# Performance work log

Hardware: AMD Instinct MI355X
Metric: run time of the kernel (lower is better)

## Reference

```python
import jax, jax.numpy as jnp
from jax import lax
import numpy as np

B, S, D_CTX = 32, 384, 300
H = 600            # hard-coded in the torch module (torch.zeros([1, 600]))
IN = D_CTX + 3     # context + 3-dim BIO tag embedding


def setup_inputs() -> dict:
    key = jax.random.key(0)
    ks = jax.random.split(key, 12)
    sc = lambda *sh: 1.0 / np.sqrt(sh[-1])
    return {
        "context": jax.random.normal(ks[0], (B, S, D_CTX), jnp.float32),
        "answer_tags": jax.random.randint(ks[1], (B, 1, S), 0, 3),
        "bio_emb": jax.random.normal(ks[2], (3, 3), jnp.float32),
        # GRUCell params (torch layout: W_ih [3H, IN], W_hh [3H, H])
        "W_ih": jax.random.normal(ks[3], (3 * H, IN), jnp.float32) * sc(3 * H, IN),
        "b_ih": jax.random.normal(ks[4], (3 * H,), jnp.float32) * 0.01,
        "W_hh": jax.random.normal(ks[5], (3 * H, H), jnp.float32) * sc(3 * H, H),
        "b_hh": jax.random.normal(ks[6], (3 * H,), jnp.float32) * 0.01,
        "W_lin": jax.random.normal(ks[7], (2 * H, 2 * H), jnp.float32) * sc(2 * H, 2 * H),
        "b_lin": jnp.zeros((2 * H,), jnp.float32),
        "W_g": jax.random.normal(ks[8], (2 * H, 4 * H), jnp.float32) * sc(2 * H, 4 * H),
        "b_g": jnp.zeros((2 * H,), jnp.float32),
        "W_f": jax.random.normal(ks[9], (2 * H, 4 * H), jnp.float32) * sc(2 * H, 4 * H),
        "b_f": jnp.zeros((2 * H,), jnp.float32),
    }


def _gru_scan(xs, W_ih, b_ih, W_hh, b_hh):
    # xs: [T, IN]; hidden carries across ALL steps (the torch code never resets
    # the hidden state between batch elements -- faithful quirk).
    gi_all = xs @ W_ih.T + b_ih            # [T, 3H] precomputed input projections

    def step(h, gi):
        gh = h @ W_hh.T + b_hh             # [3H]
        ir, iz, inn = jnp.split(gi, 3)
        hr, hz, hn = jnp.split(gh, 3)
        r = jax.nn.sigmoid(ir + hr)
        z = jax.nn.sigmoid(iz + hz)
        n = jnp.tanh(inn + r * hn)
        h_new = (1.0 - z) * n + z * h
        return h_new, h_new

    h0 = jnp.zeros((H,), xs.dtype)
    h_last, hs = lax.scan(step, h0, gi_all)
    return h_last, hs                      # [H], [T, H]


def reference(context, answer_tags, bio_emb, W_ih, b_ih, W_hh, b_hh,
              W_lin, b_lin, W_g, b_g, W_f, b_f):
    b, s, _ = context.shape
    tags = bio_emb[answer_tags[:, 0, :]]                    # [B, S, 3]
    emb = jnp.concatenate([tags, context], axis=-1)          # [B, S, IN]

    # Forward direction: one continuous scan over all B*S steps (hidden not reset).
    h_f, fwd = _gru_scan(emb.reshape(b * s, -1), W_ih, b_ih, W_hh, b_hh)
    forward_states = fwd.reshape(b, s, H)

    # Backward direction: words reversed within each batch element; the torch
    # code stores backward_states[b, w] = state after processing word S-1-w.
    h_b, bwd = _gru_scan(emb[:, ::-1, :].reshape(b * s, -1), W_ih, b_ih, W_hh, b_hh)
    backward_states = bwd.reshape(b, s, H)

    all_h = jnp.concatenate([forward_states, backward_states], axis=-1)  # [B,S,2H]

    # calc_attention: the inner state_idx loop OVERWRITES attn[b,:,:] each
    # iteration, so only the LAST state (index S-1) survives, broadcast over S.
    hs = all_h[:, -1, :]                                     # [B, 2H]
    q = hs @ W_lin.T + b_lin                                 # [B, 2H]
    scores = jax.nn.softmax(jnp.einsum('bd,bsd->bs', q, all_h), axis=-1)
    ctx = jnp.einsum('bs,bsd->bd', scores, all_h)            # [B, 2H]
    cat = jnp.concatenate([ctx, hs], axis=-1)                # [B, 4H]
    g = jax.nn.sigmoid(cat @ W_g.T + b_g)
    f = jnp.tanh(cat @ W_f.T + b_f)
    gated = g * f + (1.0 - g) * hs                           # [B, 2H]
    attn = jnp.broadcast_to(gated[:, None, :], (b, s, 2 * H))

    final = jnp.concatenate([h_f, h_b])[None, :]             # [1, 2H]
    return final, attn
```

## Files before the change

kernel.cpp:

```cpp
#include <hip/hip_runtime.h>
#include <math.h>

#define TT    12288
#define HH    600
#define GG    1800
#define INP   303
#define INP_P 304
#define BB    32
#define SS    384
#define D2    1200
#define D4    2400

#define NWG  75
#define JPW  8
#define ROWS 24

#define SENT 0xAAAAAAAAu

#define EMB_OFF    0ull
#define WP_OFF     3735552ull
#define GI_OFF     4282752ull
#define HS_OFF     26403808ull
#define Q_OFF      26442208ull
#define CTX_OFF    26480608ull
#define GATED_OFF  26519008ull
#define P_OFF      0ull

__global__ void build_emb(const float* __restrict__ ctx, const int* __restrict__ tags,
                          const float* __restrict__ bio, float* __restrict__ emb) {
    int idx = blockIdx.x * 256 + threadIdx.x;
    if (idx >= TT * INP_P) return;
    int row = idx / INP_P;
    int c = idx - row * INP_P;
    float v;
    if (c < 3)        v = bio[tags[row] * 3 + c];
    else if (c < INP) v = ctx[(size_t)row * 300 + (c - 3)];
    else              v = 0.f;
    emb[idx] = v;
}

__global__ void pad_wih(const float* __restrict__ W, float* __restrict__ Wp) {
    int idx = blockIdx.x * 256 + threadIdx.x;
    if (idx >= GG * INP_P) return;
    int r = idx / INP_P, c = idx - r * INP_P;
    Wp[idx] = (c < INP) ? W[(size_t)r * INP + c] : 0.f;
}

__global__ __launch_bounds__(256) void gemm_gi(const float* __restrict__ A,
                                               const float* __restrict__ Bw,
                                               const float* __restrict__ bias,
                                               float* __restrict__ C) {
    __shared__ float As[16][68];
    __shared__ float Bs[16][68];
    const int tid = threadIdx.x;
    const int bm = blockIdx.x, bn = blockIdx.y;
    const int tx = tid & 15, ty = tid >> 4;
    const int lm = tid >> 2;
    const int lk = (tid & 3) * 4;
    const int gbase = bn * 64;
    float acc[4][4] = {};
    for (int k0 = 0; k0 < INP_P; k0 += 16) {
        float4 av = *(const float4*)(A + (size_t)(bm * 64 + lm) * INP_P + k0 + lk);
        int grow = gbase + lm;
        float4 bv = make_float4(0.f, 0.f, 0.f, 0.f);
        if (grow < GG) bv = *(const float4*)(Bw + (size_t)grow * INP_P + k0 + lk);
        As[lk + 0][lm] = av.x; As[lk + 1][lm] = av.y; As[lk + 2][lm] = av.z; As[lk + 3][lm] = av.w;
        Bs[lk + 0][lm] = bv.x; Bs[lk + 1][lm] = bv.y; Bs[lk + 2][lm] = bv.z; Bs[lk + 3][lm] = bv.w;
        __syncthreads();
#pragma unroll
        for (int kk = 0; kk < 16; ++kk) {
            float4 a4 = *(const float4*)&As[kk][tx * 4];
            float4 b4 = *(const float4*)&Bs[kk][ty * 4];
            acc[0][0] += a4.x * b4.x; acc[0][1] += a4.x * b4.y; acc[0][2] += a4.x * b4.z; acc[0][3] += a4.x * b4.w;
            acc[1][0] += a4.y * b4.x; acc[1][1] += a4.y * b4.y; acc[1][2] += a4.y * b4.z; acc[1][3] += a4.y * b4.w;
            acc[2][0] += a4.z * b4.x; acc[2][1] += a4.z * b4.y; acc[2][2] += a4.z * b4.z; acc[2][3] += a4.z * b4.w;
            acc[3][0] += a4.w * b4.x; acc[3][1] += a4.w * b4.y; acc[3][2] += a4.w * b4.z; acc[3][3] += a4.w * b4.w;
        }
        __syncthreads();
    }
    int g0 = gbase + ty * 4;
    if (g0 < GG) {
        float4 bi4 = *(const float4*)(bias + g0);
#pragma unroll
        for (int i = 0; i < 4; ++i) {
            float4 v = make_float4(acc[i][0] + bi4.x, acc[i][1] + bi4.y,
                                   acc[i][2] + bi4.z, acc[i][3] + bi4.w);
            *(float4*)(C + (size_t)(bm * 64 + tx * 4 + i) * GG + g0) = v;
        }
    }
}

__global__ __launch_bounds__(256) void gru_scan(const float* __restrict__ gi,
                                                const float* __restrict__ Whh,
                                                const float* __restrict__ bhh,
                                                float* __restrict__ out) {
    __shared__ __align__(16) float h_lds[600];
    __shared__ __align__(16) float partials[720];
    __shared__ float gi_lds[ROWS];
    __shared__ float bhh_lds[ROWS];

    const int tid = threadIdx.x;
    const int chain = blockIdx.x / NWG;
    const int wg = blockIdx.x % NWG;
    const int j0 = wg * JPW;

    float* statesOut = out + 1200 + (size_t)chain * TT * 600;
    unsigned* statesU = (unsigned*)statesOut;

    const int rg = (tid < 240) ? tid / 30 : 0;
    const int cc = (tid < 240) ? tid % 30 : 0;
    float4 wreg[3][5];
    if (tid < 240) {
#pragma unroll
        for (int g = 0; g < 3; ++g) {
            int row = g * 600 + j0 + rg;
#pragma unroll
            for (int u = 0; u < 5; ++u)
                wreg[g][u] = *(const float4*)(Whh + (size_t)row * 600 + cc * 20 + u * 4);
        }
    }
    if (tid < ROWS) {
        int row = (tid >> 3) * 600 + j0 + (tid & 7);
        bhh_lds[tid] = bhh[row];
    }

    const int w2 = tid + 512;
    const int w2c = (w2 < 600) ? w2 : 0;
    int si = 0, bi = 0;

    for (int t = 0; t < TT; ++t) {
        float gi_reg = 0.f;
        if (tid < ROWS) {
            int gi_row = (chain == 0) ? t : (bi * SS + (SS - 1) - si);
            gi_reg = gi[(size_t)gi_row * GG + (tid >> 3) * 600 + j0 + (tid & 7)];
        }
        if (t == 0) {
            h_lds[tid] = 0.f;
            h_lds[tid + 256] = 0.f;
            if (w2 < 600) h_lds[w2] = 0.f;
        } else {
            const unsigned* hu = statesU + (size_t)(t - 1) * 600;
            unsigned b0 = SENT, b1 = SENT, b2 = (w2 < 600) ? SENT : 0u;
            for (;;) {
                if (b0 == SENT) b0 = __hip_atomic_load(hu + tid,       __ATOMIC_RELAXED, __HIP_MEMORY_SCOPE_AGENT);
                if (b1 == SENT) b1 = __hip_atomic_load(hu + tid + 256, __ATOMIC_RELAXED, __HIP_MEMORY_SCOPE_AGENT);
                if (b2 == SENT) b2 = __hip_atomic_load(hu + w2c,       __ATOMIC_RELAXED, __HIP_MEMORY_SCOPE_AGENT);
                if (b0 != SENT && b1 != SENT && b2 != SENT) break;
                __builtin_amdgcn_s_sleep(1);
            }
            h_lds[tid] = __uint_as_float(b0);
            h_lds[tid + 256] = __uint_as_float(b1);
            if (w2 < 600) h_lds[w2] = __uint_as_float(b2);
        }
        __syncthreads();
        if (tid < 240) {
            const float4* h4p = (const float4*)h_lds;
            float a0 = 0.f, a1 = 0.f, a2 = 0.f;
#pragma unroll
            for (int u = 0; u < 5; ++u) {
                float4 h4 = h4p[cc * 5 + u];
                a0 += wreg[0][u].x * h4.x + wreg[0][u].y * h4.y + wreg[0][u].z * h4.z + wreg[0][u].w * h4.w;
                a1 += wreg[1][u].x * h4.x + wreg[1][u].y * h4.y + wreg[1][u].z * h4.z + wreg[1][u].w * h4.w;
                a2 += wreg[2][u].x * h4.x + wreg[2][u].y * h4.y + wreg[2][u].z * h4.z + wreg[2][u].w * h4.w;
            }
            partials[tid] = a0;
            partials[240 + tid] = a1;
            partials[480 + tid] = a2;
        }
        if (tid < ROWS) gi_lds[tid] = gi_reg;
        __syncthreads();
        if (tid < 64) {
            float s = 0.f;
            if (tid < 24) {
                const float2* p2 = (const float2*)(partials + (tid >> 3) * 240 + (tid & 7) * 30);
                float s0 = 0.f, s1 = 0.f;
#pragma unroll
                for (int c = 0; c < 15; c += 3) {
                    float2 x = p2[c], y = p2[c + 1], z = p2[c + 2];
                    s0 += x.x + x.y; s1 += y.x + y.y; s0 += z.x + z.y;
                }
                s = s0 + s1 + bhh_lds[tid];
            }
            float dz = __shfl(s, tid + 8);
            float dn = __shfl(s, tid + 16);
            if (tid < JPW) {
                int jg = j0 + tid;
                float r = 1.f / (1.f + __expf(-(gi_lds[tid] + s)));
                float z = 1.f / (1.f + __expf(-(gi_lds[8 + tid] + dz)));
                float x = gi_lds[16 + tid] + r * dn;
                float e = __expf(-2.f * fabsf(x));
                float n = copysignf((1.f - e) / (1.f + e), x);
                float hnew = (1.f - z) * n + z * h_lds[jg];
                if (__float_as_uint(hnew) == SENT) hnew = __uint_as_float(SENT + 1u);
                __hip_atomic_store(statesU + (size_t)t * 600 + jg, __float_as_uint(hnew),
                                   __ATOMIC_RELAXED, __HIP_MEMORY_SCOPE_AGENT);
                if (t == TT - 1) out[chain * 600 + jg] = hnew;
            }
        }
        if (++si == SS) { si = 0; ++bi; }
    }
}

__global__ __launch_bounds__(256) void attn_qs(const float* __restrict__ Wlin,
                                               const float* __restrict__ blin,
                                               const float* __restrict__ outp,
                                               float* __restrict__ ws) {
    __shared__ float hs_lds[1200];
    const int bi = blockIdx.x, ob = blockIdx.y * 60, tid = threadIdx.x;
    const float* fwdS = outp + 1200;
    const float* bwdS = outp + 1200 + (size_t)TT * 600;
    size_t row = (size_t)(bi * SS + SS - 1) * 600;
    for (int k = tid; k < 600; k += 256) {
        hs_lds[k] = fwdS[row + k];
        hs_lds[600 + k] = bwdS[row + k];
    }
    __syncthreads();
    if (blockIdx.y == 0) {
        float* ws_hs = ws + HS_OFF;
        for (int k = tid; k < 1200; k += 256) ws_hs[bi * 1200 + k] = hs_lds[k];
    }
    float* ws_q = ws + Q_OFF;
    const int wave = tid >> 6, lane = tid & 63;
    for (int i = 0; i < 15; ++i) {
        int o = ob + wave * 15 + i;
        const float* wr = Wlin + (size_t)o * 1200;
        float acc = 0.f;
        for (int k = lane; k < 1200; k += 64) acc += hs_lds[k] * wr[k];
        for (int off = 32; off > 0; off >>= 1) acc += __shfl_down(acc, off);
        if (lane == 0) ws_q[bi * 1200 + o] = acc + blin[o];
    }
}

__global__ __launch_bounds__(256) void attn_logits(const float* __restrict__ outp,
                                                   float* __restrict__ ws) {
    __shared__ float q_lds[1200];
    __shared__ float p_lds[SS];
    __shared__ float red[8];
    const int bi = blockIdx.x, tid = threadIdx.x;
    const float* fwdS = outp + 1200;
    const float* bwdS = outp + 1200 + (size_t)TT * 600;
    const float* ws_q = ws + Q_OFF;
    for (int k = tid; k < 1200; k += 256) q_lds[k] = ws_q[bi * 1200 + k];
    __syncthreads();
    const int wave = tid >> 6, lane = tid & 63;
    for (int s = wave; s < SS; s += 4) {
        size_t base = (size_t)(bi * SS + s) * 600;
        float acc = 0.f;
        for (int k = lane; k < 600; k += 64)
            acc += q_lds[k] * fwdS[base + k] + q_lds[600 + k] * bwdS[base + k];
        for (int off = 32; off > 0; off >>= 1) acc += __shfl_down(acc, off);
        if (lane == 0) p_lds[s] = acc;
    }
    __syncthreads();
    float m = -1e30f;
    for (int i = tid; i < SS; i += 256) m = fmaxf(m, p_lds[i]);
    for (int off = 32; off > 0; off >>= 1) m = fmaxf(m, __shfl_down(m, off));
    if (lane == 0) red[wave] = m;
    __syncthreads();
    m = fmaxf(fmaxf(red[0], red[1]), fmaxf(red[2], red[3]));
    float ssum = 0.f;
    for (int i = tid; i < SS; i += 256) ssum += expf(p_lds[i] - m);
    for (int off = 32; off > 0; off >>= 1) ssum += __shfl_down(ssum, off);
    __syncthreads();
    if (lane == 0) red[wave] = ssum;
    __syncthreads();
    ssum = red[0] + red[1] + red[2] + red[3];
    float inv = 1.f / ssum;
    float* ws_p = ws + P_OFF;
    for (int i = tid; i < SS; i += 256) ws_p[bi * SS + i] = expf(p_lds[i] - m) * inv;
}

__global__ __launch_bounds__(256) void attn_ctxv(const float* __restrict__ outp,
                                                 float* __restrict__ ws) {
    __shared__ float p_lds[SS];
    const int bi = blockIdx.x, d0 = blockIdx.y * 240, tid = threadIdx.x;
    const float* ws_p = ws + P_OFF;
    for (int k = tid; k < SS; k += 256) p_lds[k] = ws_p[bi * SS + k];
    __syncthreads();
    if (tid >= 240) return;
    const int d = d0 + tid;
    const float* fwdS = outp + 1200;
    const float* bwdS = outp + 1200 + (size_t)TT * 600;
    const float* Sb = (d < 600) ? (fwdS + d) : (bwdS + d - 600);
    size_t rbase = (size_t)bi * SS * 600;
    float a0 = 0.f, a1 = 0.f, a2 = 0.f, a3 = 0.f;
#pragma unroll 4
    for (int s = 0; s < SS; s += 4) {
        a0 += p_lds[s + 0] * Sb[rbase + (size_t)(s + 0) * 600];
        a1 += p_lds[s + 1] * Sb[rbase + (size_t)(s + 1) * 600];
        a2 += p_lds[s + 2] * Sb[rbase + (size_t)(s + 2) * 600];
        a3 += p_lds[s + 3] * Sb[rbase + (size_t)(s + 3) * 600];
    }
    (ws + CTX_OFF)[bi * 1200 + d] = (a0 + a1) + (a2 + a3);
}

__global__ __launch_bounds__(256) void attn_gate(const float* __restrict__ Wg,
                                                 const float* __restrict__ bg,
                                                 const float* __restrict__ Wf,
                                                 const float* __restrict__ bf,
                                                 float* __restrict__ ws) {
    __shared__ float cat_lds[2400];
    const int bi = blockIdx.x, ob = blockIdx.y * 60, tid = threadIdx.x;
    const float* ws_ctx = ws + CTX_OFF;
    const float* ws_hs = ws + HS_OFF;
    for (int k = tid; k < 1200; k += 256) {
        cat_lds[k] = ws_ctx[bi * 1200 + k];
        cat_lds[1200 + k] = ws_hs[bi * 1200 + k];
    }
    __syncthreads();
    float* ws_g = ws + GATED_OFF;
    const int wave = tid >> 6, lane = tid & 63;
    for (int i = 0; i < 15; ++i) {
        int o = ob + wave * 15 + i;
        const float* wg = Wg + (size_t)o * D4;
        const float* wf = Wf + (size_t)o * D4;
        float ag = 0.f, af = 0.f;
        for (int k = lane; k < D4; k += 64) {
            float c = cat_lds[k];
            ag += c * wg[k];
            af += c * wf[k];
        }
        for (int off = 32; off > 0; off >>= 1) {
            ag += __shfl_down(ag, off);
            af += __shfl_down(af, off);
        }
        if (lane == 0) {
            float g = 1.f / (1.f + expf(-(ag + bg[o])));
            float f = tanhf(af + bf[o]);
            ws_g[bi * 1200 + o] = g * f + (1.f - g) * cat_lds[1200 + o];
        }
    }
}

__global__ void bcast_attn(const float* __restrict__ ws, float* __restrict__ outp) {
    int idx = blockIdx.x * 256 + threadIdx.x;
    const float4* g4 = (const float4*)(ws + GATED_OFF);
    float4* o4 = (float4*)outp;
    int row = idx / 300;
    int d4 = idx - row * 300;
    int bi = row / SS;
    o4[300 + idx] = g4[bi * 300 + d4];
}

extern "C" void kernel_launch(void* const* d_in, const int* in_sizes, int n_in,
                              void* d_out, int out_size, void* d_ws, size_t ws_size,
                              hipStream_t stream) {
    const float* ctx   = (const float*)d_in[0];
    const int*   tags  = (const int*)d_in[1];
    const float* bio   = (const float*)d_in[2];
    const float* W_ih  = (const float*)d_in[3];
    const float* b_ih  = (const float*)d_in[4];
    const float* W_hh  = (const float*)d_in[5];
    const float* b_hh  = (const float*)d_in[6];
    const float* W_lin = (const float*)d_in[7];
    const float* b_lin = (const float*)d_in[8];
    const float* W_g   = (const float*)d_in[9];
    const float* b_g   = (const float*)d_in[10];
    const float* W_f   = (const float*)d_in[11];
    const float* b_f   = (const float*)d_in[12];
    float* out = (float*)d_out;
    float* ws  = (float*)d_ws;

    hipMemsetAsync(out + 1200, 0xAA, (size_t)2 * TT * 600 * sizeof(float), stream);

    build_emb<<<(TT * INP_P + 255) / 256, 256, 0, stream>>>(ctx, tags, bio, ws + EMB_OFF);
    pad_wih<<<(GG * INP_P + 255) / 256, 256, 0, stream>>>(W_ih, ws + WP_OFF);
    gemm_gi<<<dim3(TT / 64, 29), 256, 0, stream>>>(ws + EMB_OFF, ws + WP_OFF, b_ih, ws + GI_OFF);
    gru_scan<<<2 * NWG, 256, 0, stream>>>(ws + GI_OFF, W_hh, b_hh, out);
    attn_qs<<<dim3(BB, 20), 256, 0, stream>>>(W_lin, b_lin, out, ws);
    attn_logits<<<BB, 256, 0, stream>>>(out, ws);
    attn_ctxv<<<dim3(BB, 5), 256, 0, stream>>>(out, ws);
    attn_gate<<<dim3(BB, 20), 256, 0, stream>>>(W_g, b_g, W_f, b_f, ws);
    bcast_attn<<<14400, 256, 0, stream>>>(ws, out);
}
```

Measured before the change: 23.51 ms.

## Restructure GRU scan to half-wave rows with shuffle reduction and double-buffered h

Result: slower. 35.68 ms (+51.8%).

```diff
diff --git a/kernel.cpp b/kernel.cpp
--- a/kernel.cpp
+++ b/kernel.cpp
@@ -13,7 +13,6 @@
 
 #define NWG  75
 #define JPW  8
-#define ROWS 24
 
 #define SENT 0xAAAAAAAAu
 
@@ -90,112 +89,98 @@
     }
 }
 
-__global__ __launch_bounds__(256) void gru_scan(const float* __restrict__ gi,
-                                                const float* __restrict__ Whh,
-                                                const float* __restrict__ bhh,
-                                                float* __restrict__ out) {
-    __shared__ __align__(16) float h_lds[600];
-    __shared__ __align__(16) float partials[720];
-    __shared__ float gi_lds[ROWS];
-    __shared__ float bhh_lds[ROWS];
+__global__ __launch_bounds__(256, 1) void gru_scan(const float* __restrict__ gi,
+                                                   const float* __restrict__ Whh,
+                                                   const float* __restrict__ bhh,
+                                                   float* __restrict__ out) {
+    __shared__ __align__(16) float h_lds[2][640];
 
     const int tid = threadIdx.x;
     const int chain = blockIdx.x / NWG;
     const int wg = blockIdx.x % NWG;
     const int j0 = wg * JPW;
+    const int wave = tid >> 6;
+    const int lane = tid & 63;
+    const int half = lane >> 5;
+    const int s = lane & 31;
+    const int j = wave * 2 + half;
+    const int jg = j0 + j;
 
     float* statesOut = out + 1200 + (size_t)chain * TT * 600;
     unsigned* statesU = (unsigned*)statesOut;
 
-    const int rg = (tid < 240) ? tid / 30 : 0;
-    const int cc = (tid < 240) ? tid % 30 : 0;
     float4 wreg[3][5];
-    if (tid < 240) {
-#pragma unroll
-        for (int g = 0; g < 3; ++g) {
-            int row = g * 600 + j0 + rg;
-#pragma unroll
-            for (int u = 0; u < 5; ++u)
-                wreg[g][u] = *(const float4*)(Whh + (size_t)row * 600 + cc * 20 + u * 4);
-        }
-    }
-    if (tid < ROWS) {
-        int row = (tid >> 3) * 600 + j0 + (tid & 7);
-        bhh_lds[tid] = bhh[row];
-    }
-
-    const int w2 = tid + 512;
-    const int w2c = (w2 < 600) ? w2 : 0;
+#pragma unroll
+    for (int g = 0; g < 3; ++g) {
+        const float* wr = Whh + (size_t)(g * 600 + jg) * 600;
+#pragma unroll
+        for (int u = 0; u < 5; ++u) {
+            int col = s * 20 + u * 4;
+            if (s < 30) wreg[g][u] = *(const float4*)(wr + col);
+            else        wreg[g][u] = make_float4(0.f, 0.f, 0.f, 0.f);
+        }
+    }
+    float b_r = 0.f, b_z = 0.f, b_n = 0.f;
+    if (s == 0) { b_r = bhh[jg]; b_z = bhh[600 + jg]; b_n = bhh[1200 + jg]; }
+
+    for (int i = tid; i < 1280; i += 256) h_lds[0][i] = 0.f;
+    __syncthreads();
+
+    float h_own = 0.f;
     int si = 0, bi = 0;
 
     for (int t = 0; t < TT; ++t) {
-        float gi_reg = 0.f;
-        if (tid < ROWS) {
+        float gr = 0.f, gz = 0.f, gn = 0.f;
+        if (s == 0) {
             int gi_row = (chain == 0) ? t : (bi * SS + (SS - 1) - si);
-            gi_reg = gi[(size_t)gi_row * GG + (tid >> 3) * 600 + j0 + (tid & 7)];
-        }
-        if (t == 0) {
-            h_lds[tid] = 0.f;
-            h_lds[tid + 256] = 0.f;
-            if (w2 < 600) h_lds[w2] = 0.f;
-        } else {
-            const unsigned* hu = statesU + (size_t)(t - 1) * 600;
-            unsigned b0 = SENT, b1 = SENT, b2 = (w2 < 600) ? SENT : 0u;
-            for (;;) {
-                if (b0 == SENT) b0 = __hip_atomic_load(hu + tid,       __ATOMIC_RELAXED, __HIP_MEMORY_SCOPE_AGENT);
-                if (b1 == SENT) b1 = __hip_atomic_load(hu + tid + 256, __ATOMIC_RELAXED, __HIP_MEMORY_SCOPE_AGENT);
-                if (b2 == SENT) b2 = __hip_atomic_load(hu + w2c,       __ATOMIC_RELAXED, __HIP_MEMORY_SCOPE_AGENT);
-                if (b0 != SENT && b1 != SENT && b2 != SENT) break;
-                __builtin_amdgcn_s_sleep(1);
+            const float* gp = gi + (size_t)gi_row * GG + jg;
+            gr = gp[0]; gz = gp[600]; gn = gp[1200];
+        }
+        const int slot = t & 1;
+        if (t > 0) {
+            if (tid < 150) {
+                const unsigned* hu = statesU + (size_t)(t - 1) * 600 + tid * 4;
+                unsigned u0, u1, u2, u3;
+                for (;;) {
+                    u0 = __hip_atomic_load(hu + 0, __ATOMIC_RELAXED, __HIP_MEMORY_SCOPE_AGENT);
+                    u1 = __hip_atomic_load(hu + 1, __ATOMIC_RELAXED, __HIP_MEMORY_SCOPE_AGENT);
+                    u2 = __hip_atomic_load(hu + 2, __ATOMIC_RELAXED, __HIP_MEMORY_SCOPE_AGENT);
+                    u3 = __hip_atomic_load(hu + 3, __ATOMIC_RELAXED, __HIP_MEMORY_SCOPE_AGENT);
+                    if (u0 != SENT && u1 != SENT && u2 != SENT && u3 != SENT) break;
+                }
+                float4 hv = make_float4(__uint_as_float(u0), __uint_as_float(u1),
+                                        __uint_as_float(u2), __uint_as_float(u3));
+                ((float4*)h_lds[slot])[tid] = hv;
             }
-            h_lds[tid] = __uint_as_float(b0);
-            h_lds[tid + 256] = __uint_as_float(b1);
-            if (w2 < 600) h_lds[w2] = __uint_as_float(b2);
-        }
-        __syncthreads();
-        if (tid < 240) {
-            const float4* h4p = (const float4*)h_lds;
-            float a0 = 0.f, a1 = 0.f, a2 = 0.f;
-#pragma unroll
-            for (int u = 0; u < 5; ++u) {
-                float4 h4 = h4p[cc * 5 + u];
-                a0 += wreg[0][u].x * h4.x + wreg[0][u].y * h4.y + wreg[0][u].z * h4.z + wreg[0][u].w * h4.w;
-                a1 += wreg[1][u].x * h4.x + wreg[1][u].y * h4.y + wreg[1][u].z * h4.z + wreg[1][u].w * h4.w;
-                a2 += wreg[2][u].x * h4.x + wreg[2][u].y * h4.y + wreg[2][u].z * h4.z + wreg[2][u].w * h4.w;
-            }
-            partials[tid] = a0;
-            partials[240 + tid] = a1;
-            partials[480 + tid] = a2;
-        }
-        if (tid < ROWS) gi_lds[tid] = gi_reg;
-        __syncthreads();
-        if (tid < 64) {
-            float s = 0.f;
-            if (tid < 24) {
-                const float2* p2 = (const float2*)(partials + (tid >> 3) * 240 + (tid & 7) * 30);
-                float s0 = 0.f, s1 = 0.f;
-#pragma unroll
-                for (int c = 0; c < 15; c += 3) {
-                    float2 x = p2[c], y = p2[c + 1], z = p2[c + 2];
-                    s0 += x.x + x.y; s1 += y.x + y.y; s0 += z.x + z.y;
-                }
-                s = s0 + s1 + bhh_lds[tid];
-            }
-            float dz = __shfl(s, tid + 8);
-            float dn = __shfl(s, tid + 16);
-            if (tid < JPW) {
-                int jg = j0 + tid;
-                float r = 1.f / (1.f + __expf(-(gi_lds[tid] + s)));
-                float z = 1.f / (1.f + __expf(-(gi_lds[8 + tid] + dz)));
-                float x = gi_lds[16 + tid] + r * dn;
-                float e = __expf(-2.f * fabsf(x));
-                float n = copysignf((1.f - e) / (1.f + e), x);
-                float hnew = (1.f - z) * n + z * h_lds[jg];
-                if (__float_as_uint(hnew) == SENT) hnew = __uint_as_float(SENT + 1u);
-                __hip_atomic_store(statesU + (size_t)t * 600 + jg, __float_as_uint(hnew),
-                                   __ATOMIC_RELAXED, __HIP_MEMORY_SCOPE_AGENT);
-                if (t == TT - 1) out[chain * 600 + jg] = hnew;
-            }
+            __syncthreads();
+        }
+        const float4* h4 = (const float4*)h_lds[slot];
+        float a0 = 0.f, a1 = 0.f, a2 = 0.f;
+#pragma unroll
+        for (int u = 0; u < 5; ++u) {
+            float4 hv = h4[s * 5 + u];
+            a0 += wreg[0][u].x * hv.x + wreg[0][u].y * hv.y + wreg[0][u].z * hv.z + wreg[0][u].w * hv.w;
+            a1 += wreg[1][u].x * hv.x + wreg[1][u].y * hv.y + wreg[1][u].z * hv.z + wreg[1][u].w * hv.w;
+            a2 += wreg[2][u].x * hv.x + wreg[2][u].y * hv.y + wreg[2][u].z * hv.z + wreg[2][u].w * hv.w;
+        }
+#pragma unroll
+        for (int off = 16; off > 0; off >>= 1) {
+            a0 += __shfl_down(a0, off, 32);
+            a1 += __shfl_down(a1, off, 32);
+            a2 += __shfl_down(a2, off, 32);
+        }
+        if (s == 0) {
+            float r = 1.f / (1.f + __expf(-(gr + a0 + b_r)));
+            float z = 1.f / (1.f + __expf(-(gz + a1 + b_z)));
+            float x = gn + r * (a2 + b_n);
+            float e = __expf(-2.f * fabsf(x));
+            float n = copysignf((1.f - e) / (1.f + e), x);
+            float hnew = (1.f - z) * n + z * h_own;
+            if (__float_as_uint(hnew) == SENT) hnew = __uint_as_float(SENT + 1u);
+            __hip_atomic_store(statesU + (size_t)t * 600 + jg, __float_as_uint(hnew),
+                               __ATOMIC_RELAXED, __HIP_MEMORY_SCOPE_AGENT);
+            h_own = hnew;
+            if (t == TT - 1) out[chain * 600 + jg] = hnew;
         }
         if (++si == SS) { si = 0; ++bi; }
     }
```
